# Kernel optimization log

Hardware: AMD Instinct MI355X
Metric: run time of the kernel (lower is better)

Reference implementation:

```python
import jax, jax.numpy as jnp
import numpy as np
import math

T, B = 512, 32
QD, SD, H, NH = 128, 256, 512, 8
NQ, NS, NSUB = 30000, 400, 8
DKEY = QD + 2 * SD      # 640
DVAL = 4 * SD + QD      # 1152
P = H + 2 * SD + QD     # 1152 (pred_in_feature)
DH = H // NH            # 64
NEG = -1e32


def _layernorm(x, g, b, eps=1e-5):
    mu = jnp.mean(x, axis=-1, keepdims=True)
    var = jnp.mean((x - mu) ** 2, axis=-1, keepdims=True)
    return (x - mu) * jax.lax.rsqrt(var + eps) * g + b


def setup_inputs() -> dict:
    key = jax.random.key(0)
    ks = iter(jax.random.split(key, 48))
    def nrm(shape, scale=0.05):
        return (scale * jax.random.normal(next(ks), shape)).astype(jnp.float32)
    inp = {}
    inp['ans'] = jax.random.randint(next(ks), (T, B), 1, 5, dtype=jnp.int32)
    inp['correct_ans'] = jax.random.randint(next(ks), (T, B), 1, 5, dtype=jnp.int32)
    inp['labels'] = jax.random.randint(next(ks), (T, B), 0, 2, dtype=jnp.int32)
    inp['mask'] = jnp.ones((T, B), jnp.float32)
    inp['q_ids'] = jax.random.randint(next(ks), (T, B), 0, NQ, dtype=jnp.int32)
    inp['subject_ids'] = jax.random.randint(next(ks), (T, B, NSUB), 0, NS, dtype=jnp.int32)
    inp['subject_mask'] = (jax.random.uniform(next(ks), (T, B, NSUB)) < 0.7).astype(jnp.float32)
    inp['Eq'] = nrm((NQ, QD)); inp['Es'] = nrm((NS, SD))
    inp['Ea'] = nrm((4, SD)); inp['El'] = nrm((2, SD))
    inp['Wq'] = nrm((H, DKEY)); inp['bq'] = jnp.zeros((H,), jnp.float32)
    inp['Wk'] = nrm((H, DKEY)); inp['bk'] = jnp.zeros((H,), jnp.float32)
    inp['Wv'] = nrm((H, DVAL)); inp['bv'] = jnp.zeros((H,), jnp.float32)
    inp['Wo'] = nrm((H, H)); inp['bo'] = jnp.zeros((H,), jnp.float32)
    inp['ln1_g'] = jnp.ones((H,), jnp.float32); inp['ln1_b'] = jnp.zeros((H,), jnp.float32)
    inp['W1'] = nrm((H, H)); inp['b1'] = jnp.zeros((H,), jnp.float32)
    inp['W2'] = nrm((H, H)); inp['b2'] = jnp.zeros((H,), jnp.float32)
    inp['ln2_g'] = jnp.ones((H,), jnp.float32); inp['ln2_b'] = jnp.zeros((H,), jnp.float32)
    inp['gammas'] = jnp.zeros((NH, 1, 1), jnp.float32)
    inp['L1W'] = nrm((P, P)); inp['L1b'] = jnp.zeros((P,), jnp.float32)
    inp['L2W'] = nrm((P, P)); inp['L2b'] = jnp.zeros((P,), jnp.float32)
    inp['OW'] = nrm((1, P)); inp['Ob'] = jnp.zeros((1,), jnp.float32)
    return inp


def _forward(ans, correct_ans, labels, q_ids, subject_ids,
             mask, subject_mask, Eq, Es, Ea, El,
             Wq, bq, Wk, bk, Wv, bv, Wo, bo, ln1_g, ln1_b,
             W1, b1, W2, b2, ln2_g, ln2_b, gammas,
             L1W, L1b, L2W, L2b, OW, Ob):
    m3 = mask[:, :, None]                                   # [T,B,1]
    subjects = jnp.sum(Es[subject_ids] * subject_mask[..., None], axis=2)   # [T,B,SD]
    questions = Eq[q_ids]                                   # [T,B,QD]
    ans_embed = Ea[ans - 1] * m3
    ca_embed = Ea[correct_ans - 1]
    lab_embed = El[labels] * m3
    query = jnp.concatenate([questions, subjects, ca_embed], axis=-1)       # [T,B,DKEY]
    value = jnp.concatenate([lab_embed, ans_embed, ca_embed, questions, subjects], axis=-1)  # [T,B,DVAL]
    # note: original applies q_linear to kk and k_linear to qq (qq==kk==query here); akt=True => no pos-embed
    q = (query @ Wq.T + bq).reshape(T, B, NH, DH).transpose(1, 2, 0, 3)     # [B,NH,T,DH]
    k = (query @ Wk.T + bk).reshape(T, B, NH, DH).transpose(1, 2, 0, 3)
    v = (value @ Wv.T + bv).reshape(T, B, NH, DH).transpose(1, 2, 0, 3)
    scores = jnp.einsum('bhqd,bhkd->bhqk', q, k) / math.sqrt(DH)            # [B,NH,T,T]
    scores = jnp.where(mask.T[:, None, None, :] == 0, NEG, scores)
    # exponential distance decay (Softplus-gamma), applied AFTER the key-pad fill as in the original
    idx = jnp.arange(T)
    pe = jnp.sqrt(jnp.abs(idx[None, :] - idx[:, None]).astype(jnp.float32)) # [T,T]
    total_effect = jnp.clip(jnp.exp(pe[None] * (-jax.nn.softplus(gammas))), 1e-5, 1e5)  # [NH,T,T]
    scores = scores * total_effect[None]
    causal_bad = jnp.triu(jnp.ones((T, T), bool))            # upper incl. diagonal is masked
    scores = jnp.where(causal_bad, NEG, scores)
    scores = jax.nn.softmax(scores, axis=-1)
    scores = scores.at[:, :, 0, :].set(0.0)                  # pad-zero first query row
    attn = jnp.einsum('bhqk,bhkd->bhqd', scores, v)
    concat = attn.transpose(2, 0, 1, 3).reshape(T, B, H)
    out = _layernorm(concat @ Wo.T + bo, ln1_g, ln1_b)
    ffn = jax.nn.relu(out @ W1.T + b1) @ W2.T + b2
    out = out + _layernorm(ffn, ln2_g, ln2_b)
    pred = jnp.concatenate([out, questions, subjects, ca_embed], axis=-1)   # [T,B,P]
    h = jax.nn.relu(pred @ L1W.T + L1b)
    h = jax.nn.relu(h @ L2W.T + L2b)
    logits = ((h + pred) @ OW.T + Ob)[..., 0]                # [T,B]
    y = labels.astype(jnp.float32)
    bce = jnp.maximum(logits, 0.0) - logits * y + jnp.log1p(jnp.exp(-jnp.abs(logits)))
    loss = jnp.mean(bce * mask) / jnp.mean(mask)
    return loss


def reference(ans, correct_ans, labels, mask, q_ids, subject_ids, subject_mask,
              Eq, Es, Ea, El, Wq, bq, Wk, bk, Wv, bv, Wo, bo, ln1_g, ln1_b,
              W1, b1, W2, b2, ln2_g, ln2_b, gammas, L1W, L1b, L2W, L2b, OW, Ob):
    return _forward(ans, correct_ans, labels, q_ids, subject_ids,
                    mask, subject_mask, Eq, Es, Ea, El,
                    Wq, bq, Wk, bk, Wv, bv, Wo, bo, ln1_g, ln1_b,
                    W1, b1, W2, b2, ln2_g, ln2_b, gammas,
                    L1W, L1b, L2W, L2b, OW, Ob)
```

## Files before the change

kernel.cpp:

```cpp
#include <hip/hip_runtime.h>
#include <math.h>

#define T_LEN 512
#define B_SZ  32
#define NHEAD 8
#define DHEAD 64
#define H_DIM 512
#define TBTOK 16384
#define P_DIM 1152
#define P_PAD 1280

typedef unsigned short ushort_t;
typedef short short8 __attribute__((ext_vector_type(8)));
typedef float f32x4 __attribute__((ext_vector_type(4)));

__device__ __forceinline__ ushort_t f2bf(float f) {
    union { float f; unsigned int u; } v; v.f = f;
    unsigned int r = v.u + 0x7fffu + ((v.u >> 16) & 1u);
    return (ushort_t)(r >> 16);
}
__device__ __forceinline__ float bf2f(ushort_t h) {
    union { unsigned int u; float f; } v; v.u = ((unsigned int)h) << 16;
    return v.f;
}
__device__ __forceinline__ void gload_lds16(const void* g, void* l) {
    __builtin_amdgcn_global_load_lds(
        (const __attribute__((address_space(1))) void*)g,
        (__attribute__((address_space(3))) void*)l, 16, 0, 0);
}

__global__ __launch_bounds__(256) void convert_weights(
    const float* __restrict__ wq, const float* __restrict__ wk,
    const float* __restrict__ wv, const float* __restrict__ wo,
    const float* __restrict__ w1, const float* __restrict__ w2,
    ushort_t* __restrict__ dst, float* __restrict__ accum)
{
    if (blockIdx.x == 0 && threadIdx.x < 2) accum[threadIdx.x] = 0.f;
    const unsigned int offs[7] = {0u, 327680u, 655360u, 1245184u, 1507328u,
                                  1769472u, 2031616u};
    unsigned int c = (blockIdx.x * 256 + threadIdx.x) * 4;
    const float* srcs[6] = {wq, wk, wv, wo, w1, w2};
    int s = 0;
#pragma unroll
    for (int i = 0; i < 5; i++) s += (c >= offs[i + 1]) ? 1 : 0;
    float4 v = *(const float4*)(srcs[s] + (c - offs[s]));
    ushort4 o;
    o.x = f2bf(v.x); o.y = f2bf(v.y); o.z = f2bf(v.z); o.w = f2bf(v.w);
    *(ushort4*)(dst + c) = o;
}

__global__ __launch_bounds__(256) void pad_weights(
    const float* __restrict__ l1, const float* __restrict__ l2,
    const float* __restrict__ L1b, const float* __restrict__ L2b,
    const float* __restrict__ OW,
    ushort_t* __restrict__ l1d, ushort_t* __restrict__ l2d,
    float* __restrict__ L1bp, float* __restrict__ L2bp, float* __restrict__ OWp)
{
    int blk = blockIdx.x;
    if (blk < 1440) {
        int o4 = (blk * 256 + threadIdx.x) * 4;
        int row = o4 / 1152;
        int col = o4 - row * 1152;
        ushort4 o; o.x = 0; o.y = 0; o.z = 0; o.w = 0;
        if (row < 1152) {
            float4 v = *(const float4*)(l1 + (size_t)row * 1152 + col);
            o.x = f2bf(v.x); o.y = f2bf(v.y); o.z = f2bf(v.z); o.w = f2bf(v.w);
        }
        *(ushort4*)(l1d + o4) = o;
    } else if (blk < 3040) {
        int o4 = ((blk - 1440) * 256 + threadIdx.x) * 4;
        int row = o4 / 1280;
        int col = o4 - row * 1280;
        ushort4 o; o.x = 0; o.y = 0; o.z = 0; o.w = 0;
        if (row < 1152 && col < 1152) {
            float4 v = *(const float4*)(l2 + (size_t)row * 1152 + col);
            o.x = f2bf(v.x); o.y = f2bf(v.y); o.z = f2bf(v.z); o.w = f2bf(v.w);
        }
        *(ushort4*)(l2d + o4) = o;
    } else {
        for (int i = threadIdx.x; i < P_PAD; i += 256) {
            L1bp[i] = (i < P_DIM) ? L1b[i] : 0.f;
            L2bp[i] = (i < P_DIM) ? L2b[i] : 0.f;
            OWp[i]  = (i < P_DIM) ? OW[i]  : 0.f;
        }
    }
}

__global__ __launch_bounds__(256) void embed_kernel(
    const int* __restrict__ ans, const int* __restrict__ cans,
    const int* __restrict__ labels, const float* __restrict__ mask,
    const int* __restrict__ qids, const int* __restrict__ sids,
    const float* __restrict__ smask,
    const float* __restrict__ Eq, const float* __restrict__ Es,
    const float* __restrict__ Ea, const float* __restrict__ El,
    ushort_t* __restrict__ pred_bf, ushort_t* __restrict__ value_bf,
    const float* __restrict__ OW, const float* __restrict__ Ob,
    float* __restrict__ lgits)
{
    __shared__ float red[4];
    int m = blockIdx.x;
    int tid = threadIdx.x;
    float mval = mask[m];
    int qid = qids[m];
    int a   = ans[m] - 1;
    int ca  = cans[m] - 1;
    int lb  = labels[m];
    ushort_t* pr = pred_bf  + (size_t)m * P_DIM;
    ushort_t* vr = value_bf + (size_t)m * P_DIM;

    float part = 0.f;
    if (tid < 128) {
        ushort_t qv = f2bf(Eq[(size_t)qid * 128 + tid]);
        pr[512 + tid] = qv;
        vr[768 + tid] = qv;
        part = bf2f(qv) * OW[512 + tid];
    }
    int d = tid;
    float s = 0.f;
#pragma unroll
    for (int j = 0; j < 8; j++) {
        int  sid = sids[m * 8 + j];
        float sm = smask[m * 8 + j];
        s += Es[(size_t)sid * 256 + d] * sm;
    }
    ushort_t sb = f2bf(s);
    pr[640 + d] = sb;
    vr[896 + d] = sb;
    ushort_t cab = f2bf(Ea[ca * 256 + d]);
    pr[896 + d] = cab;
    vr[512 + d] = cab;
    vr[256 + d] = f2bf(Ea[a * 256 + d] * mval);
    vr[0   + d] = f2bf(El[lb * 256 + d] * mval);

    part = fmaf(bf2f(sb),  OW[640 + d], part);
    part = fmaf(bf2f(cab), OW[896 + d], part);
#pragma unroll
    for (int off = 32; off >= 1; off >>= 1) part += __shfl_xor(part, off, 64);
    if ((tid & 63) == 0) red[tid >> 6] = part;
    __syncthreads();
    if (tid == 0) lgits[m] = red[0] + red[1] + red[2] + red[3] + Ob[0];
}

template<int MODE, bool RELU>
__global__ __launch_bounds__(256) void mgemm(
    const ushort_t* __restrict__ A, int lda,
    const ushort_t* __restrict__ W, int ldw,
    const float* __restrict__ bias, const float* __restrict__ bias2,
    ushort_t* __restrict__ Cb, ushort_t* __restrict__ Cb2, int ldc, int K,
    const float* __restrict__ OW, float* __restrict__ lg)
{
    __shared__ __align__(16) ushort_t As[128 * 32];
    __shared__ __align__(16) ushort_t Ws[128 * 32];
    __shared__ __align__(16) ushort_t et[4][32][72];

    const int m0 = blockIdx.x * 128;
    const int n0 = blockIdx.y * 128;
    const int tid  = threadIdx.x;
    const int wave = tid >> 6;
    const int lane = tid & 63;
    const int wm = wave & 1, wn = wave >> 1;

    f32x4 acc[4][4] = {};

    const int srow = lane >> 2;
    const int lchunk = ((((lane & 3) - ((srow >> 1) & 3)) & 3)) * 8;
    int arowA, arowB;
    if (MODE == 4) {
        int mA = m0 + wave * 32 + srow;
        int mB = mA + 16;
        arowA = ((mA & 511) << 5) + (mA >> 9);
        arowB = ((mB & 511) << 5) + (mB >> 9);
    } else {
        arowA = m0 + wave * 32 + srow;
        arowB = arowA + 16;
    }
    const ushort_t* Ag0 = A + (size_t)arowA * lda + lchunk;
    const ushort_t* Ag1 = A + (size_t)arowB * lda + lchunk;
    const ushort_t* Wg0 = W + (size_t)(n0 + wave * 32 + srow) * ldw + lchunk;
    const ushort_t* Wg1 = Wg0 + (size_t)16 * ldw;
    ushort_t* Al0 = &As[(wave * 32) * 32];
    ushort_t* Al1 = &As[(wave * 32 + 16) * 32];
    ushort_t* Wl0 = &Ws[(wave * 32) * 32];
    ushort_t* Wl1 = &Ws[(wave * 32 + 16) * 32];

    const int fr   = lane & 15;
    const int quad = lane >> 4;
    const int csw  = ((quad + ((fr >> 1) & 3)) & 3) * 8;

    for (int k0 = 0; k0 < K; k0 += 32) {
        gload_lds16(Ag0 + k0, Al0);
        gload_lds16(Ag1 + k0, Al1);
        gload_lds16(Wg0 + k0, Wl0);
        gload_lds16(Wg1 + k0, Wl1);
        __syncthreads();
        short8 af[4], wf[4];
#pragma unroll
        for (int i = 0; i < 4; i++)
            af[i] = *(const short8*)&As[(wm * 64 + i * 16 + fr) * 32 + csw];
#pragma unroll
        for (int j = 0; j < 4; j++)
            wf[j] = *(const short8*)&Ws[(wn * 64 + j * 16 + fr) * 32 + csw];
#pragma unroll
        for (int i = 0; i < 4; i++)
#pragma unroll
            for (int j = 0; j < 4; j++)
                acc[i][j] = __builtin_amdgcn_mfma_f32_16x16x32_bf16(
                    af[i], wf[j], acc[i][j], 0, 0, 0);
        __syncthreads();
    }

    const int nbase = n0 + wn * 64;
    bool side = (MODE == 5) && (nbase >= 512);
    const float* bp = side ? bias2 : bias;
    const int boff  = (MODE == 5) ? (nbase & 511) : nbase;
    const float scl = (MODE == 5 && !side) ? 0.125f : 1.f;

    const int sub8 = (lane & 7) * 8;
    const int grp  = lane >> 3;

#pragma unroll
    for (int hh = 0; hh < 2; hh++) {
        if (MODE == 4) {
#pragma unroll
            for (int i = 0; i < 4; i++)
#pragma unroll
                for (int r = 0; r < 4; r++) {
                    int rl = i * 16 + quad * 4 + r;
#pragma unroll
                    for (int j = 2 * hh; j < 2 * hh + 2; j++) {
                        int cl = j * 16 + fr;
                        float v = acc[i][j][r] + bp[boff + cl];
                        if (RELU) v = fmaxf(v, 0.f);
                        et[wave][cl - 32 * hh][rl] = f2bf(v);
                    }
                }
        } else {
#pragma unroll
            for (int i = 2 * hh; i < 2 * hh + 2; i++)
#pragma unroll
                for (int r = 0; r < 4; r++) {
                    int rl = i * 16 + quad * 4 + r;
#pragma unroll
                    for (int j = 0; j < 4; j++) {
                        int cl = j * 16 + fr;
                        float v = (acc[i][j][r] + bp[boff + cl]) * scl;
                        if (RELU) v = fmaxf(v, 0.f);
                        et[wave][rl - 32 * hh][cl] = f2bf(v);
                    }
                }
        }
#pragma unroll
        for (int rr = 0; rr < 4; rr++) {
            int rowl = rr * 8 + grp;
            short8 val = *(const short8*)&et[wave][rowl][sub8];
            if (MODE == 1) {
                int row = m0 + wm * 64 + 32 * hh + rowl;
                int col = nbase + sub8;
                *(short8*)&Cb[(size_t)row * ldc + col] = val;
            } else if (MODE == 5) {
                int row = m0 + wm * 64 + 32 * hh + rowl;
                int t = row >> 5, b = row & 31;
                int h = (nbase >> 6) & 7;
                ushort_t* base = side ? Cb2 : Cb;
                *(short8*)&base[(((size_t)(b * 8 + h)) << 15) + ((size_t)t << 6) + sub8] = val;
            } else {
                int m = m0 + wm * 64 + sub8;
                int b = m >> 9, t = m & 511;
                int h = nbase >> 6;
                int d = 32 * hh + rowl;
                *(short8*)&Cb[(((size_t)(b * 8 + h)) << 15) + ((size_t)d << 9) + t] = val;
            }
        }
    }
}

template<int MODE, bool RELU>
__global__ __launch_bounds__(512, 2) void gemm320(
    const ushort_t* __restrict__ A, int lda,
    const ushort_t* __restrict__ W, int ldw,
    const float* __restrict__ bias,
    ushort_t* __restrict__ Cb, int ldc, int K,
    const float* __restrict__ OW, float* __restrict__ lg)
{
    __shared__ __align__(16) ushort_t As2[2][2][256 * 32];
    __shared__ __align__(16) ushort_t Bs2[2][2][320 * 32];

    const int m0 = blockIdx.x * 256;
    const int n0 = blockIdx.y * 320;
    const int tid  = threadIdx.x;
    const int wave = tid >> 6;
    const int lane = tid & 63;
    const int wm = wave >> 2, wn = wave & 3;
    const int fr   = lane & 15;
    const int quad = lane >> 4;
    const int csw  = ((quad + ((fr >> 1) & 3)) & 3) * 8;

    const int slr = lane >> 2;
    const int sc  = (((lane & 3) - ((lane >> 3) & 3)) & 3) * 8;
    const ushort_t* Asrc = A + (size_t)(m0 + slr) * lda + sc;
    const ushort_t* Wsrc = W + (size_t)(n0 + slr) * ldw + sc;
    const int NT = K >> 6;

    auto stA = [&](int t, int kh) {
#pragma unroll
        for (int n = 0; n < 2; n++) {
            int rl = (wave + 8 * n) << 4;
            gload_lds16(Asrc + (size_t)rl * lda + (t * 64 + kh * 32),
                        &As2[t & 1][kh][rl * 32]);
        }
    };
    auto stB = [&](int t, int kh) {
#pragma unroll
        for (int n = 0; n < 2; n++) {
            int rl = (wave + 8 * n) << 4;
            gload_lds16(Wsrc + (size_t)rl * ldw + (t * 64 + kh * 32),
                        &Bs2[t & 1][kh][rl * 32]);
        }
        if (wave < 4) {
            int rl = (wave + 16) << 4;
            gload_lds16(Wsrc + (size_t)rl * ldw + (t * 64 + kh * 32),
                        &Bs2[t & 1][kh][rl * 32]);
        }
    };
    auto waitK = [&](int t) {
        if (t + 2 < NT) {
            if (wave < 4) asm volatile("s_waitcnt vmcnt(5)" ::: "memory");
            else          asm volatile("s_waitcnt vmcnt(4)" ::: "memory");
        } else {
            asm volatile("s_waitcnt vmcnt(0)" ::: "memory");
        }
    };

    f32x4 acc[8][5] = {};

    stA(0, 0); stB(0, 0); stA(0, 1); stB(0, 1);
    if (NT > 1) { stA(1, 0); stB(1, 0); }
    if (NT > 2) {
        if (wave < 4) asm volatile("s_waitcnt vmcnt(5)" ::: "memory");
        else          asm volatile("s_waitcnt vmcnt(4)" ::: "memory");
    } else {
        asm volatile("s_waitcnt vmcnt(0)" ::: "memory");
    }
    __builtin_amdgcn_s_barrier();

    short8 af[4], bf[5];
    for (int t = 0; t < NT; ++t) {
        const int db = t & 1;
        const ushort_t* Ar0 = &As2[db][0][0];
        const ushort_t* Ar1 = &As2[db][1][0];
        const ushort_t* Br0 = &Bs2[db][0][0];
        const ushort_t* Br1 = &Bs2[db][1][0];

#pragma unroll
        for (int i = 0; i < 4; i++)
            af[i] = *(const short8*)&Ar0[(wm * 128 + i * 16 + fr) * 32 + csw];
#pragma unroll
        for (int j = 0; j < 5; j++)
            bf[j] = *(const short8*)&Br0[(wn * 80 + j * 16 + fr) * 32 + csw];
        if (t + 1 < NT) stA(t + 1, 1);
        __builtin_amdgcn_s_barrier();
        __builtin_amdgcn_s_setprio(1);
#pragma unroll
        for (int i = 0; i < 4; i++)
#pragma unroll
            for (int j = 0; j < 5; j++)
                acc[i][j] = __builtin_amdgcn_mfma_f32_16x16x32_bf16(
                    af[i], bf[j], acc[i][j], 0, 0, 0);
        __builtin_amdgcn_s_setprio(0);
        __builtin_amdgcn_s_barrier();

#pragma unroll
        for (int i = 0; i < 4; i++)
            af[i] = *(const short8*)&Ar0[(wm * 128 + 64 + i * 16 + fr) * 32 + csw];
        if (t + 1 < NT) stB(t + 1, 1);
        __builtin_amdgcn_s_barrier();
        __builtin_amdgcn_s_setprio(1);
#pragma unroll
        for (int i = 0; i < 4; i++)
#pragma unroll
            for (int j = 0; j < 5; j++)
                acc[4 + i][j] = __builtin_amdgcn_mfma_f32_16x16x32_bf16(
                    af[i], bf[j], acc[4 + i][j], 0, 0, 0);
        __builtin_amdgcn_s_setprio(0);
        __builtin_amdgcn_s_barrier();

#pragma unroll
        for (int i = 0; i < 4; i++)
            af[i] = *(const short8*)&Ar1[(wm * 128 + i * 16 + fr) * 32 + csw];
#pragma unroll
        for (int j = 0; j < 5; j++)
            bf[j] = *(const short8*)&Br1[(wn * 80 + j * 16 + fr) * 32 + csw];
        if (t + 2 < NT) stA(t + 2, 0);
        __builtin_amdgcn_s_barrier();
        __builtin_amdgcn_s_setprio(1);
#pragma unroll
        for (int i = 0; i < 4; i++)
#pragma unroll
            for (int j = 0; j < 5; j++)
                acc[i][j] = __builtin_amdgcn_mfma_f32_16x16x32_bf16(
                    af[i], bf[j], acc[i][j], 0, 0, 0);
        __builtin_amdgcn_s_setprio(0);
        __builtin_amdgcn_s_barrier();

#pragma unroll
        for (int i = 0; i < 4; i++)
            af[i] = *(const short8*)&Ar1[(wm * 128 + 64 + i * 16 + fr) * 32 + csw];
        if (t + 2 < NT) stB(t + 2, 0);
        waitK(t);
        __builtin_amdgcn_s_barrier();
        __builtin_amdgcn_s_setprio(1);
#pragma unroll
        for (int i = 0; i < 4; i++)
#pragma unroll
            for (int j = 0; j < 5; j++)
                acc[4 + i][j] = __builtin_amdgcn_mfma_f32_16x16x32_bf16(
                    af[i], bf[j], acc[4 + i][j], 0, 0, 0);
        __builtin_amdgcn_s_setprio(0);
        __builtin_amdgcn_s_barrier();
    }

    const int nbase = n0 + wn * 80;

    if (MODE == 3) {
#pragma unroll
        for (int ii = 0; ii < 8; ii++)
#pragma unroll
            for (int r = 0; r < 4; r++) {
                int row = m0 + wm * 128 + (ii >> 2) * 64 + (ii & 3) * 16 + quad * 4 + r;
                float part = 0.f;
#pragma unroll
                for (int j = 0; j < 5; j++) {
                    int col = nbase + j * 16 + fr;
                    float v = fmaxf(acc[ii][j][r] + bias[col], 0.f);
                    part = fmaf(v, OW[col], part);
                }
                part += __shfl_xor(part, 1, 64);
                part += __shfl_xor(part, 2, 64);
                part += __shfl_xor(part, 4, 64);
                part += __shfl_xor(part, 8, 64);
                if (fr == 0) atomicAdd(&lg[row], part);
            }
        return;
    }

    ushort_t* etw = ((ushort_t*)As2) + wave * (16 * 88);
#pragma unroll
    for (int ii = 0; ii < 8; ii++) {
#pragma unroll
        for (int r = 0; r < 4; r++)
#pragma unroll
            for (int j = 0; j < 5; j++) {
                float v = acc[ii][j][r] + bias[nbase + j * 16 + fr];
                if (RELU) v = fmaxf(v, 0.f);
                etw[(quad * 4 + r) * 88 + j * 16 + fr] = f2bf(v);
            }
        int rowb = m0 + wm * 128 + (ii >> 2) * 64 + (ii & 3) * 16;
        for (int u = lane; u < 160; u += 64) {
            int rr = u / 10;
            int cc = u - rr * 10;
            short8 val = *(const short8*)&etw[rr * 88 + cc * 8];
            *(short8*)&Cb[(size_t)(rowb + rr) * ldc + nbase + cc * 8] = val;
        }
    }
}

__global__ __launch_bounds__(256) void attn_mfma(
    const ushort_t* __restrict__ qb, const ushort_t* __restrict__ kb,
    const ushort_t* __restrict__ vtb, const float* __restrict__ mask,
    const float* __restrict__ gammas, ushort_t* __restrict__ attnc)
{
    __shared__ __align__(16) ushort_t kbuf[2][64 * 64];
    __shared__ __align__(16) ushort_t vbuf[2][64 * 64];
    __shared__ __align__(16) ushort_t ps[4][16][72];
    __shared__ float decayF[512];
    __shared__ float mneg[512];

    const int bh  = blockIdx.x;
    const int b   = bh >> 3;
    const int h   = bh & 7;
    const int qt0 = (7 - blockIdx.y) * 64;
    const int tid  = threadIdx.x;
    const int wave = tid >> 6;
    const int lane = tid & 63;
    const int fr   = lane & 15;
    const int quad = lane >> 4;

    {
        float g  = gammas[h];
        float sp = (g > 20.f) ? g : log1pf(expf(g));
        for (int i = tid; i < 512; i += 256) {
            decayF[i] = fmaxf(exp2f(-sp * 1.44269504f * sqrtf((float)i)), 1e-5f)
                        * 1.44269504f;
            mneg[i]   = (mask[(size_t)i * B_SZ + b] == 0.f) ? -1e32f : 0.f;
        }
    }

    const int qr0 = qt0 + wave * 16;
    const ushort_t* qbase = qb  + ((size_t)bh << 15);
    const ushort_t* kbase = kb  + ((size_t)bh << 15);
    const ushort_t* vbase = vtb + ((size_t)bh << 15);

    short8 af0 = *(const short8*)(qbase + (size_t)(qr0 + fr) * 64 + quad * 8);
    short8 af1 = *(const short8*)(qbase + (size_t)(qr0 + fr) * 64 + 32 + quad * 8);
    const short8 ones = {0x3F80, 0x3F80, 0x3F80, 0x3F80,
                         0x3F80, 0x3F80, 0x3F80, 0x3F80};

    const int rl0 = wave * 16 + (lane >> 3);
    const int rl1 = rl0 + 8;
    const int sc0 = (((lane & 7) - rl0) & 7) * 8;
    const int sc1 = (((lane & 7) - rl1) & 7) * 8;

    auto stage = [&](int kt, int bufi) {
        gload_lds16(kbase + (size_t)(kt + rl0) * 64 + sc0, &kbuf[bufi][(wave * 16) * 64]);
        gload_lds16(kbase + (size_t)(kt + rl1) * 64 + sc1, &kbuf[bufi][(wave * 16 + 8) * 64]);
        gload_lds16(vbase + (size_t)rl0 * T_LEN + kt + sc0, &vbuf[bufi][(wave * 16) * 64]);
        gload_lds16(vbase + (size_t)rl1 * T_LEN + kt + sc1, &vbuf[bufi][(wave * 16 + 8) * 64]);
    };
    auto frag = [&](const ushort_t* buf, int row, int lchunk) -> short8 {
        return *(const short8*)&buf[row * 64 + ((lchunk + row) & 7) * 8];
    };

    stage(0, 0);

    f32x4 o[4] = {};
    f32x4 lacc = {};
    int bufi = 0;

    for (int kt0 = 0; kt0 <= qt0; kt0 += 64) {
        __syncthreads();
        if (kt0 < qt0) stage(kt0 + 64, bufi ^ 1);
        const bool diag = (kt0 == qt0);
        const ushort_t* kb_ = kbuf[bufi];
        const ushort_t* vb_ = vbuf[bufi];

        f32x4 sacc[4] = {};
#pragma unroll
        for (int j = 0; j < 4; j++) {
            int row = j * 16 + fr;
            short8 k0 = frag(kb_, row, quad);
            short8 k1 = frag(kb_, row, quad + 4);
            sacc[j] = __builtin_amdgcn_mfma_f32_16x16x32_bf16(af0, k0, sacc[j], 0, 0, 0);
            sacc[j] = __builtin_amdgcn_mfma_f32_16x16x32_bf16(af1, k1, sacc[j], 0, 0, 0);
        }

#pragma unroll
        for (int j = 0; j < 4; j++) {
            int kg = kt0 + j * 16 + fr;
            float mn = mneg[kg];
            int qgb = qr0 + quad * 4;
            if (!diag) {
                int base = qgb - kg;
#pragma unroll
                for (int r = 0; r < 4; r++) {
                    float t = fmaf(sacc[j][r], decayF[base + r], mn);
                    union { float f; unsigned u; } cv; cv.f = exp2f(t);
                    ps[wave][quad * 4 + r][j * 16 + fr] = (ushort_t)(cv.u >> 16);
                }
            } else {
#pragma unroll
                for (int r = 0; r < 4; r++) {
                    int didx = qgb + r - kg;
                    float dec = decayF[didx > 0 ? didx : 0];
                    float t = fmaf(sacc[j][r], dec, mn);
                    if (didx <= 0) t = -1e32f;
                    union { float f; unsigned u; } cv; cv.f = exp2f(t);
                    ps[wave][quad * 4 + r][j * 16 + fr] = (ushort_t)(cv.u >> 16);
                }
            }
        }
        short8 pf0 = *(const short8*)&ps[wave][fr][quad * 8];
        short8 pf1 = *(const short8*)&ps[wave][fr][32 + quad * 8];
        lacc = __builtin_amdgcn_mfma_f32_16x16x32_bf16(pf0, ones, lacc, 0, 0, 0);
        lacc = __builtin_amdgcn_mfma_f32_16x16x32_bf16(pf1, ones, lacc, 0, 0, 0);
#pragma unroll
        for (int j2 = 0; j2 < 4; j2++) {
            int row = j2 * 16 + fr;
            short8 v0 = frag(vb_, row, quad);
            short8 v1 = frag(vb_, row, quad + 4);
            o[j2] = __builtin_amdgcn_mfma_f32_16x16x32_bf16(pf0, v0, o[j2], 0, 0, 0);
            o[j2] = __builtin_amdgcn_mfma_f32_16x16x32_bf16(pf1, v1, o[j2], 0, 0, 0);
        }
        bufi ^= 1;
    }

#pragma unroll
    for (int r = 0; r < 4; r++) {
        int qg = qr0 + quad * 4 + r;
        float linv = (qg == 0) ? 0.f : 1.f / lacc[r];
#pragma unroll
        for (int j2 = 0; j2 < 4; j2++)
            ps[wave][quad * 4 + r][j2 * 16 + fr] = f2bf(o[j2][r] * linv);
    }
    const int sub8 = (lane & 7) * 8;
    const int grp  = lane >> 3;
#pragma unroll
    for (int half = 0; half < 2; half++) {
        int rowl = half * 8 + grp;
        short8 val = *(const short8*)&ps[wave][rowl][sub8];
        int qg = qr0 + rowl;
        *(short8*)&attnc[((size_t)qg * B_SZ + b) * H_DIM + h * DHEAD + sub8] = val;
    }
}

__global__ __launch_bounds__(256) void ln1_kernel(
    const ushort_t* __restrict__ X, const float* __restrict__ g,
    const float* __restrict__ bta, ushort_t* __restrict__ Yb)
{
    int m    = blockIdx.x * 4 + (threadIdx.x >> 6);
    int lane = threadIdx.x & 63;
    int c0   = lane * 8;
    const ushort_t* xr = X + (size_t)m * H_DIM + c0;
    float x[8];
    float s = 0.f, ss = 0.f;
    short8 xv = *(const short8*)xr;
#pragma unroll
    for (int i = 0; i < 8; i++) {
        x[i] = bf2f((ushort_t)xv[i]);
        s += x[i]; ss += x[i] * x[i];
    }
#pragma unroll
    for (int off = 32; off >= 1; off >>= 1) {
        s  += __shfl_xor(s,  off, 64);
        ss += __shfl_xor(ss, off, 64);
    }
    float mu  = s * (1.f / 512.f);
    float var = ss * (1.f / 512.f) - mu * mu;
    float rs  = rsqrtf(var + 1e-5f);
    ushort_t yb[8];
#pragma unroll
    for (int i = 0; i < 8; i++)
        yb[i] = f2bf((x[i] - mu) * rs * g[c0 + i] + bta[c0 + i]);
    *(short8*)(Yb + (size_t)m * H_DIM + c0) = *(short8*)&yb[0];
}

__global__ __launch_bounds__(256) void ln2_kernel(
    const ushort_t* __restrict__ X, const float* __restrict__ g,
    const float* __restrict__ bta, const ushort_t* __restrict__ res,
    ushort_t* __restrict__ pred_bf, const float* __restrict__ OW,
    float* __restrict__ lg)
{
    int m    = blockIdx.x * 4 + (threadIdx.x >> 6);
    int lane = threadIdx.x & 63;
    int c0   = lane * 8;
    const ushort_t* xr = X + (size_t)m * H_DIM + c0;
    float x[8];
    float s = 0.f, ss = 0.f;
    short8 xv = *(const short8*)xr;
#pragma unroll
    for (int i = 0; i < 8; i++) {
        x[i] = bf2f((ushort_t)xv[i]);
        s += x[i]; ss += x[i] * x[i];
    }
#pragma unroll
    for (int off = 32; off >= 1; off >>= 1) {
        s  += __shfl_xor(s,  off, 64);
        ss += __shfl_xor(ss, off, 64);
    }
    float mu  = s * (1.f / 512.f);
    float var = ss * (1.f / 512.f) - mu * mu;
    float rs  = rsqrtf(var + 1e-5f);
    short8 rv = *(const short8*)(res + (size_t)m * H_DIM + c0);
    ushort_t yb[8];
    float part = 0.f;
#pragma unroll
    for (int i = 0; i < 8; i++) {
        float v = (x[i] - mu) * rs * g[c0 + i] + bta[c0 + i] + bf2f((ushort_t)rv[i]);
        yb[i] = f2bf(v);
        part = fmaf(v, OW[c0 + i], part);
    }
    *(short8*)(pred_bf + (size_t)m * P_DIM + c0) = *(short8*)&yb[0];
#pragma unroll
    for (int off = 32; off >= 1; off >>= 1) part += __shfl_xor(part, off, 64);
    if (lane == 0) lg[m] += part;
}

__global__ __launch_bounds__(256) void bce_kernel(
    const float* __restrict__ lg, const int* __restrict__ labels,
    const float* __restrict__ mask, float* __restrict__ accum)
{
    int m    = blockIdx.x * 256 + threadIdx.x;
    int lane = threadIdx.x & 63;
    float l  = lg[m];
    float y  = (float)labels[m];
    float mv = mask[m];
    float a  = (fmaxf(l, 0.f) - l * y + log1pf(expf(-fabsf(l)))) * mv;
#pragma unroll
    for (int off = 32; off >= 1; off >>= 1) {
        a  += __shfl_xor(a,  off, 64);
        mv += __shfl_xor(mv, off, 64);
    }
    if (lane == 0) {
        atomicAdd(accum,     a);
        atomicAdd(accum + 1, mv);
    }
}

__global__ void finalize_kernel(const float* __restrict__ accum, float* __restrict__ out)
{
    out[0] = accum[0] / accum[1];
}

extern "C" void kernel_launch(void* const* d_in, const int* in_sizes, int n_in,
                              void* d_out, int out_size, void* d_ws, size_t ws_size,
                              hipStream_t stream)
{
    (void)in_sizes; (void)n_in; (void)out_size;
    const int*   ans    = (const int*)  d_in[0];
    const int*   cans   = (const int*)  d_in[1];
    const int*   labels = (const int*)  d_in[2];
    const float* mask   = (const float*)d_in[3];
    const int*   qids   = (const int*)  d_in[4];
    const int*   sids   = (const int*)  d_in[5];
    const float* smask  = (const float*)d_in[6];
    const float* Eq     = (const float*)d_in[7];
    const float* Es     = (const float*)d_in[8];
    const float* Ea     = (const float*)d_in[9];
    const float* El     = (const float*)d_in[10];
    const float* Wq     = (const float*)d_in[11];
    const float* bq     = (const float*)d_in[12];
    const float* Wk     = (const float*)d_in[13];
    const float* bk     = (const float*)d_in[14];
    const float* Wv     = (const float*)d_in[15];
    const float* bv     = (const float*)d_in[16];
    const float* Wo     = (const float*)d_in[17];
    const float* bo     = (const float*)d_in[18];
    const float* ln1_g  = (const float*)d_in[19];
    const float* ln1_b  = (const float*)d_in[20];
    const float* W1     = (const float*)d_in[21];
    const float* b1     = (const float*)d_in[22];
    const float* W2     = (const float*)d_in[23];
    const float* b2     = (const float*)d_in[24];
    const float* ln2_g  = (const float*)d_in[25];
    const float* ln2_b  = (const float*)d_in[26];
    const float* gammas = (const float*)d_in[27];
    const float* L1W    = (const float*)d_in[28];
    const float* L1b    = (const float*)d_in[29];
    const float* L2W    = (const float*)d_in[30];
    const float* L2b    = (const float*)d_in[31];
    const float* OW     = (const float*)d_in[32];
    const float* Ob     = (const float*)d_in[33];
    float* out = (float*)d_out;

    const size_t U = (size_t)TBTOK * 64;
    if (ws_size < 42 * U * sizeof(float)) return;
    float* ws = (float*)d_ws;
    ushort_t* wtb      = (ushort_t*)(ws);
    ushort_t* pred_bf  = (ushort_t*)(ws + 3 * U);
    ushort_t* value_bf = (ushort_t*)(ws + 12 * U);
    ushort_t* qb       = (ushort_t*)(ws + 21 * U);
    ushort_t* kb       = (ushort_t*)(ws + 25 * U);
    ushort_t* vtb      = (ushort_t*)(ws + 29 * U);
    ushort_t* attnc_bf = (ushort_t*)(ws + 33 * U);
    ushort_t* x1_bf    = (ushort_t*)(ws + 12 * U);
    ushort_t* out1_bf  = (ushort_t*)(ws + 24 * U);
    ushort_t* f1_bf    = (ushort_t*)(ws + 28 * U);
    ushort_t* f2_bf    = (ushort_t*)(ws + 32 * U);
    ushort_t* h1_bf    = (ushort_t*)(ws + 12 * U);
    float*    lgits    = ws + 41 * U;
    float*    accum    = lgits + TBTOK;
    float*    OWp      = accum + 2;
    float*    L1bp     = OWp + P_PAD;
    float*    L2bp     = L1bp + P_PAD;

    ushort_t* wqk_b = wtb + 0;
    ushort_t* wv_b  = wtb + 655360;
    ushort_t* wo_b  = wtb + 1245184;
    ushort_t* w1_b  = wtb + 1507328;
    ushort_t* w2_b  = wtb + 1769472;
    ushort_t* l1_b  = wtb + 2031616;
    ushort_t* l2_b  = wtb + 3506176;

    convert_weights<<<1984, 256, 0, stream>>>(Wq, Wk, Wv, Wo, W1, W2, wtb, accum);
    pad_weights<<<3041, 256, 0, stream>>>(L1W, L2W, L1b, L2b, OW,
                                          l1_b, l2_b, L1bp, L2bp, OWp);
    embed_kernel<<<TBTOK, 256, 0, stream>>>(ans, cans, labels, mask, qids, sids,
                                            smask, Eq, Es, Ea, El, pred_bf, value_bf,
                                            OW, Ob, lgits);
    mgemm<5,false><<<dim3(TBTOK/128, 8), 256, 0, stream>>>(
        pred_bf + 512, P_DIM, wqk_b, 640, bq, bk, qb, kb, 0, 640, nullptr, nullptr);
    mgemm<4,false><<<dim3(TBTOK/128, 4), 256, 0, stream>>>(
        value_bf, P_DIM, wv_b, P_DIM, bv, nullptr, vtb, nullptr, 0, P_DIM, nullptr, nullptr);
    attn_mfma<<<dim3(B_SZ * NHEAD, 8), 256, 0, stream>>>(
        qb, kb, vtb, mask, gammas, attnc_bf);
    mgemm<1,false><<<dim3(TBTOK/128, 4), 256, 0, stream>>>(
        attnc_bf, H_DIM, wo_b, H_DIM, bo, nullptr, x1_bf, nullptr, H_DIM, H_DIM, nullptr, nullptr);
    ln1_kernel<<<TBTOK/4, 256, 0, stream>>>(x1_bf, ln1_g, ln1_b, out1_bf);
    mgemm<1,true><<<dim3(TBTOK/128, 4), 256, 0, stream>>>(
        out1_bf, H_DIM, w1_b, H_DIM, b1, nullptr, f1_bf, nullptr, H_DIM, H_DIM, nullptr, nullptr);
    mgemm<1,false><<<dim3(TBTOK/128, 4), 256, 0, stream>>>(
        f1_bf, H_DIM, w2_b, H_DIM, b2, nullptr, f2_bf, nullptr, H_DIM, H_DIM, nullptr, nullptr);
    ln2_kernel<<<TBTOK/4, 256, 0, stream>>>(f2_bf, ln2_g, ln2_b, out1_bf, pred_bf, OW, lgits);
    gemm320<1,true><<<dim3(TBTOK/256, P_PAD/320), 512, 0, stream>>>(
        pred_bf, P_DIM, l1_b, P_DIM, L1bp, h1_bf, P_PAD, P_DIM, nullptr, nullptr);
    gemm320<3,true><<<dim3(TBTOK/256, P_PAD/320), 512, 0, stream>>>(
        h1_bf, P_PAD, l2_b, P_PAD, L2bp, nullptr, 0, P_PAD, OWp, lgits);
    bce_kernel<<<TBTOK/256, 256, 0, stream>>>(lgits, labels, mask, accum);
    finalize_kernel<<<1, 1, 0, stream>>>(accum, out);
}
```

Measured before the change: 443.6 us.

## Replace simple 128x128 GEMMs with templated double-buffered 256-row pipelined GEMM

Generalises the pipelined 256xN gemm320 kernel into a template gemm4p parameterised by column tiles, and routes the QK, V, Wo, FFN and prediction-head GEMMs through it instead of the single-buffered 128x128 mgemm. The new kernel prefetches K tiles with vmcnt-based waits, uses setprio around MFMA bursts, and adds epilogues for the Q/K head-split layout and the transposed V layout. This aims to hide global-load latency and raise MFMA utilisation. The trade-off is fewer blocks per GEMM (64x4 grids), which can leave CUs idle, plus higher register and LDS pressure.

Measured after the change: 425.3 us. 1.04x faster.

```diff
diff --git a/kernel.cpp b/kernel.cpp
--- a/kernel.cpp
+++ b/kernel.cpp
@@ -141,152 +141,20 @@
     if (tid == 0) lgits[m] = red[0] + red[1] + red[2] + red[3] + Ob[0];
 }
 
-template<int MODE, bool RELU>
-__global__ __launch_bounds__(256) void mgemm(
+template<int JC, int MODE, bool RELU>
+__global__ __launch_bounds__(512, 2) void gemm4p(
     const ushort_t* __restrict__ A, int lda,
     const ushort_t* __restrict__ W, int ldw,
     const float* __restrict__ bias, const float* __restrict__ bias2,
     ushort_t* __restrict__ Cb, ushort_t* __restrict__ Cb2, int ldc, int K,
     const float* __restrict__ OW, float* __restrict__ lg)
 {
-    __shared__ __align__(16) ushort_t As[128 * 32];
-    __shared__ __align__(16) ushort_t Ws[128 * 32];
-    __shared__ __align__(16) ushort_t et[4][32][72];
-
-    const int m0 = blockIdx.x * 128;
-    const int n0 = blockIdx.y * 128;
-    const int tid  = threadIdx.x;
-    const int wave = tid >> 6;
-    const int lane = tid & 63;
-    const int wm = wave & 1, wn = wave >> 1;
-
-    f32x4 acc[4][4] = {};
-
-    const int srow = lane >> 2;
-    const int lchunk = ((((lane & 3) - ((srow >> 1) & 3)) & 3)) * 8;
-    int arowA, arowB;
-    if (MODE == 4) {
-        int mA = m0 + wave * 32 + srow;
-        int mB = mA + 16;
-        arowA = ((mA & 511) << 5) + (mA >> 9);
-        arowB = ((mB & 511) << 5) + (mB >> 9);
-    } else {
-        arowA = m0 + wave * 32 + srow;
-        arowB = arowA + 16;
-    }
-    const ushort_t* Ag0 = A + (size_t)arowA * lda + lchunk;
-    const ushort_t* Ag1 = A + (size_t)arowB * lda + lchunk;
-    const ushort_t* Wg0 = W + (size_t)(n0 + wave * 32 + srow) * ldw + lchunk;
-    const ushort_t* Wg1 = Wg0 + (size_t)16 * ldw;
-    ushort_t* Al0 = &As[(wave * 32) * 32];
-    ushort_t* Al1 = &As[(wave * 32 + 16) * 32];
-    ushort_t* Wl0 = &Ws[(wave * 32) * 32];
-    ushort_t* Wl1 = &Ws[(wave * 32 + 16) * 32];
-
-    const int fr   = lane & 15;
-    const int quad = lane >> 4;
-    const int csw  = ((quad + ((fr >> 1) & 3)) & 3) * 8;
-
-    for (int k0 = 0; k0 < K; k0 += 32) {
-        gload_lds16(Ag0 + k0, Al0);
-        gload_lds16(Ag1 + k0, Al1);
-        gload_lds16(Wg0 + k0, Wl0);
-        gload_lds16(Wg1 + k0, Wl1);
-        __syncthreads();
-        short8 af[4], wf[4];
-#pragma unroll
-        for (int i = 0; i < 4; i++)
-            af[i] = *(const short8*)&As[(wm * 64 + i * 16 + fr) * 32 + csw];
-#pragma unroll
-        for (int j = 0; j < 4; j++)
-            wf[j] = *(const short8*)&Ws[(wn * 64 + j * 16 + fr) * 32 + csw];
-#pragma unroll
-        for (int i = 0; i < 4; i++)
-#pragma unroll
-            for (int j = 0; j < 4; j++)
-                acc[i][j] = __builtin_amdgcn_mfma_f32_16x16x32_bf16(
-                    af[i], wf[j], acc[i][j], 0, 0, 0);
-        __syncthreads();
-    }
-
-    const int nbase = n0 + wn * 64;
-    bool side = (MODE == 5) && (nbase >= 512);
-    const float* bp = side ? bias2 : bias;
-    const int boff  = (MODE == 5) ? (nbase & 511) : nbase;
-    const float scl = (MODE == 5 && !side) ? 0.125f : 1.f;
-
-    const int sub8 = (lane & 7) * 8;
-    const int grp  = lane >> 3;
-
-#pragma unroll
-    for (int hh = 0; hh < 2; hh++) {
-        if (MODE == 4) {
-#pragma unroll
-            for (int i = 0; i < 4; i++)
-#pragma unroll
-                for (int r = 0; r < 4; r++) {
-                    int rl = i * 16 + quad * 4 + r;
-#pragma unroll
-                    for (int j = 2 * hh; j < 2 * hh + 2; j++) {
-                        int cl = j * 16 + fr;
-                        float v = acc[i][j][r] + bp[boff + cl];
-                        if (RELU) v = fmaxf(v, 0.f);
-                        et[wave][cl - 32 * hh][rl] = f2bf(v);
-                    }
-                }
-        } else {
-#pragma unroll
-            for (int i = 2 * hh; i < 2 * hh + 2; i++)
-#pragma unroll
-                for (int r = 0; r < 4; r++) {
-                    int rl = i * 16 + quad * 4 + r;
-#pragma unroll
-                    for (int j = 0; j < 4; j++) {
-                        int cl = j * 16 + fr;
-                        float v = (acc[i][j][r] + bp[boff + cl]) * scl;
-                        if (RELU) v = fmaxf(v, 0.f);
-                        et[wave][rl - 32 * hh][cl] = f2bf(v);
-                    }
-                }
-        }
-#pragma unroll
-        for (int rr = 0; rr < 4; rr++) {
-            int rowl = rr * 8 + grp;
-            short8 val = *(const short8*)&et[wave][rowl][sub8];
-            if (MODE == 1) {
-                int row = m0 + wm * 64 + 32 * hh + rowl;
-                int col = nbase + sub8;
-                *(short8*)&Cb[(size_t)row * ldc + col] = val;
-            } else if (MODE == 5) {
-                int row = m0 + wm * 64 + 32 * hh + rowl;
-                int t = row >> 5, b = row & 31;
-                int h = (nbase >> 6) & 7;
-                ushort_t* base = side ? Cb2 : Cb;
-                *(short8*)&base[(((size_t)(b * 8 + h)) << 15) + ((size_t)t << 6) + sub8] = val;
-            } else {
-                int m = m0 + wm * 64 + sub8;
-                int b = m >> 9, t = m & 511;
-                int h = nbase >> 6;
-                int d = 32 * hh + rowl;
-                *(short8*)&Cb[(((size_t)(b * 8 + h)) << 15) + ((size_t)d << 9) + t] = val;
-            }
-        }
-    }
-}
-
-template<int MODE, bool RELU>
-__global__ __launch_bounds__(512, 2) void gemm320(
-    const ushort_t* __restrict__ A, int lda,
-    const ushort_t* __restrict__ W, int ldw,
-    const float* __restrict__ bias,
-    ushort_t* __restrict__ Cb, int ldc, int K,
-    const float* __restrict__ OW, float* __restrict__ lg)
-{
+    constexpr int BN = JC * 64;
     __shared__ __align__(16) ushort_t As2[2][2][256 * 32];
-    __shared__ __align__(16) ushort_t Bs2[2][2][320 * 32];
+    __shared__ __align__(16) ushort_t Bs2[2][2][BN * 32];
 
     const int m0 = blockIdx.x * 256;
-    const int n0 = blockIdx.y * 320;
+    const int n0 = blockIdx.y * BN;
     const int tid  = threadIdx.x;
     const int wave = tid >> 6;
     const int lane = tid & 63;
@@ -297,7 +165,15 @@
 
     const int slr = lane >> 2;
     const int sc  = (((lane & 3) - ((lane >> 3) & 3)) & 3) * 8;
-    const ushort_t* Asrc = A + (size_t)(m0 + slr) * lda + sc;
+    const ushort_t* Asrc;
+    size_t aRS;
+    if (MODE == 4) {
+        Asrc = A + ((size_t)(((m0 & 511) + slr) << 5) + (m0 >> 9)) * lda + sc;
+        aRS  = (size_t)32 * lda;
+    } else {
+        Asrc = A + (size_t)(m0 + slr) * lda + sc;
+        aRS  = (size_t)lda;
+    }
     const ushort_t* Wsrc = W + (size_t)(n0 + slr) * ldw + sc;
     const int NT = K >> 6;
 
@@ -305,45 +181,43 @@
 #pragma unroll
         for (int n = 0; n < 2; n++) {
             int rl = (wave + 8 * n) << 4;
-            gload_lds16(Asrc + (size_t)rl * lda + (t * 64 + kh * 32),
+            gload_lds16(Asrc + (size_t)rl * aRS + (t * 64 + kh * 32),
                         &As2[t & 1][kh][rl * 32]);
         }
     };
     auto stB = [&](int t, int kh) {
 #pragma unroll
-        for (int n = 0; n < 2; n++) {
+        for (int n = 0; n < JC / 2; n++) {
             int rl = (wave + 8 * n) << 4;
             gload_lds16(Wsrc + (size_t)rl * ldw + (t * 64 + kh * 32),
                         &Bs2[t & 1][kh][rl * 32]);
         }
-        if (wave < 4) {
-            int rl = (wave + 16) << 4;
-            gload_lds16(Wsrc + (size_t)rl * ldw + (t * 64 + kh * 32),
-                        &Bs2[t & 1][kh][rl * 32]);
+        if (JC & 1) {
+            if (wave < 4) {
+                int rl = (wave + 8 * (JC / 2)) << 4;
+                gload_lds16(Wsrc + (size_t)rl * ldw + (t * 64 + kh * 32),
+                            &Bs2[t & 1][kh][rl * 32]);
+            }
         }
     };
-    auto waitK = [&](int t) {
-        if (t + 2 < NT) {
+    auto waitSteady = [&]() {
+        if (JC == 2)      asm volatile("s_waitcnt vmcnt(3)" ::: "memory");
+        else if (JC == 4) asm volatile("s_waitcnt vmcnt(4)" ::: "memory");
+        else {
             if (wave < 4) asm volatile("s_waitcnt vmcnt(5)" ::: "memory");
             else          asm volatile("s_waitcnt vmcnt(4)" ::: "memory");
-        } else {
-            asm volatile("s_waitcnt vmcnt(0)" ::: "memory");
         }
     };
 
-    f32x4 acc[8][5] = {};
+    f32x4 acc[8][JC] = {};
 
     stA(0, 0); stB(0, 0); stA(0, 1); stB(0, 1);
     if (NT > 1) { stA(1, 0); stB(1, 0); }
-    if (NT > 2) {
-        if (wave < 4) asm volatile("s_waitcnt vmcnt(5)" ::: "memory");
-        else          asm volatile("s_waitcnt vmcnt(4)" ::: "memory");
-    } else {
-        asm volatile("s_waitcnt vmcnt(0)" ::: "memory");
-    }
+    if (NT > 2) waitSteady();
+    else        asm volatile("s_waitcnt vmcnt(0)" ::: "memory");
     __builtin_amdgcn_s_barrier();
 
-    short8 af[4], bf[5];
+    short8 af[4], bf[JC];
     for (int t = 0; t < NT; ++t) {
         const int db = t & 1;
         const ushort_t* Ar0 = &As2[db][0][0];
@@ -355,15 +229,15 @@
         for (int i = 0; i < 4; i++)
             af[i] = *(const short8*)&Ar0[(wm * 128 + i * 16 + fr) * 32 + csw];
 #pragma unroll
-        for (int j = 0; j < 5; j++)
-            bf[j] = *(const short8*)&Br0[(wn * 80 + j * 16 + fr) * 32 + csw];
+        for (int j = 0; j < JC; j++)
+            bf[j] = *(const short8*)&Br0[(wn * (JC * 16) + j * 16 + fr) * 32 + csw];
         if (t + 1 < NT) stA(t + 1, 1);
         __builtin_amdgcn_s_barrier();
         __builtin_amdgcn_s_setprio(1);
 #pragma unroll
         for (int i = 0; i < 4; i++)
 #pragma unroll
-            for (int j = 0; j < 5; j++)
+            for (int j = 0; j < JC; j++)
                 acc[i][j] = __builtin_amdgcn_mfma_f32_16x16x32_bf16(
                     af[i], bf[j], acc[i][j], 0, 0, 0);
         __builtin_amdgcn_s_setprio(0);
@@ -378,7 +252,7 @@
 #pragma unroll
         for (int i = 0; i < 4; i++)
 #pragma unroll
-            for (int j = 0; j < 5; j++)
+            for (int j = 0; j < JC; j++)
                 acc[4 + i][j] = __builtin_amdgcn_mfma_f32_16x16x32_bf16(
                     af[i], bf[j], acc[4 + i][j], 0, 0, 0);
         __builtin_amdgcn_s_setprio(0);
@@ -388,15 +262,15 @@
         for (int i = 0; i < 4; i++)
             af[i] = *(const short8*)&Ar1[(wm * 128 + i * 16 + fr) * 32 + csw];
 #pragma unroll
-        for (int j = 0; j < 5; j++)
-            bf[j] = *(const short8*)&Br1[(wn * 80 + j * 16 + fr) * 32 + csw];
+        for (int j = 0; j < JC; j++)
+            bf[j] = *(const short8*)&Br1[(wn * (JC * 16) + j * 16 + fr) * 32 + csw];
         if (t + 2 < NT) stA(t + 2, 0);
         __builtin_amdgcn_s_barrier();
         __builtin_amdgcn_s_setprio(1);
 #pragma unroll
         for (int i = 0; i < 4; i++)
 #pragma unroll
-            for (int j = 0; j < 5; j++)
+            for (int j = 0; j < JC; j++)
                 acc[i][j] = __builtin_amdgcn_mfma_f32_16x16x32_bf16(
                     af[i], bf[j], acc[i][j], 0, 0, 0);
         __builtin_amdgcn_s_setprio(0);
@@ -406,20 +280,21 @@
         for (int i = 0; i < 4; i++)
             af[i] = *(const short8*)&Ar1[(wm * 128 + 64 + i * 16 + fr) * 32 + csw];
         if (t + 2 < NT) stB(t + 2, 0);
-        waitK(t);
+        if (t + 2 < NT) waitSteady();
+        else            asm volatile("s_waitcnt vmcnt(0)" ::: "memory");
         __builtin_amdgcn_s_barrier();
         __builtin_amdgcn_s_setprio(1);
 #pragma unroll
         for (int i = 0; i < 4; i++)
 #pragma unroll
-            for (int j = 0; j < 5; j++)
+            for (int j = 0; j < JC; j++)
                 acc[4 + i][j] = __builtin_amdgcn_mfma_f32_16x16x32_bf16(
                     af[i], bf[j], acc[4 + i][j], 0, 0, 0);
         __builtin_amdgcn_s_setprio(0);
         __builtin_amdgcn_s_barrier();
     }
 
-    const int nbase = n0 + wn * 80;
+    const int nbase = n0 + wn * (JC * 16);
 
     if (MODE == 3) {
 #pragma unroll
@@ -429,7 +304,7 @@
                 int row = m0 + wm * 128 + (ii >> 2) * 64 + (ii & 3) * 16 + quad * 4 + r;
                 float part = 0.f;
 #pragma unroll
-                for (int j = 0; j < 5; j++) {
+                for (int j = 0; j < JC; j++) {
                     int col = nbase + j * 16 + fr;
                     float v = fmaxf(acc[ii][j][r] + bias[col], 0.f);
                     part = fmaf(v, OW[col], part);
@@ -443,23 +318,89 @@
         return;
     }
 
-    ushort_t* etw = ((ushort_t*)As2) + wave * (16 * 88);
-#pragma unroll
-    for (int ii = 0; ii < 8; ii++) {
-#pragma unroll
-        for (int r = 0; r < 4; r++)
-#pragma unroll
-            for (int j = 0; j < 5; j++) {
-                float v = acc[ii][j][r] + bias[nbase + j * 16 + fr];
-                if (RELU) v = fmaxf(v, 0.f);
-                etw[(quad * 4 + r) * 88 + j * 16 + fr] = f2bf(v);
+    if (MODE == 5) {
+        bool side = (nbase >= 512);
+        const float* bp = side ? bias2 : bias;
+        const int boff  = nbase & 511;
+        const float scl = side ? 1.f : 0.125f;
+        ushort_t* base  = side ? Cb2 : Cb;
+        const int h = (nbase >> 6) & 7;
+        ushort_t* etw = ((ushort_t*)As2) + wave * (16 * 72);
+#pragma unroll
+        for (int ii = 0; ii < 8; ii++) {
+#pragma unroll
+            for (int r = 0; r < 4; r++)
+#pragma unroll
+                for (int j = 0; j < 4; j++) {
+                    float v = (acc[ii][j][r] + bp[boff + j * 16 + fr]) * scl;
+                    etw[(quad * 4 + r) * 72 + j * 16 + fr] = f2bf(v);
+                }
+            int rowb = m0 + wm * 128 + (ii >> 2) * 64 + (ii & 3) * 16;
+#pragma unroll
+            for (int u = lane; u < 128; u += 64) {
+                int rr = u >> 3, cc = (u & 7) * 8;
+                int row = rowb + rr;
+                int tq = row >> 5, b = row & 31;
+                short8 val = *(const short8*)&etw[rr * 72 + cc];
+                *(short8*)&base[(((size_t)(b * 8 + h)) << 15) + ((size_t)tq << 6) + cc] = val;
             }
-        int rowb = m0 + wm * 128 + (ii >> 2) * 64 + (ii & 3) * 16;
-        for (int u = lane; u < 160; u += 64) {
-            int rr = u / 10;
-            int cc = u - rr * 10;
-            short8 val = *(const short8*)&etw[rr * 88 + cc * 8];
-            *(short8*)&Cb[(size_t)(rowb + rr) * ldc + nbase + cc * 8] = val;
+        }
+        return;
+    }
+
+    if (MODE == 4) {
+        ushort_t* etw = ((ushort_t*)As2) + wave * (32 * 72);
+        const int h = nbase >> 6;
+        const int dbase = nbase & 63;
+#pragma unroll
+        for (int mh = 0; mh < 2; mh++) {
+#pragma unroll
+            for (int i = 0; i < 4; i++)
+#pragma unroll
+                for (int r = 0; r < 4; r++) {
+                    int rl = i * 16 + quad * 4 + r;
+#pragma unroll
+                    for (int j = 0; j < 2; j++) {
+                        int cl = j * 16 + fr;
+                        float v = acc[mh * 4 + i][j][r] + bias[nbase + cl];
+                        etw[cl * 72 + rl] = f2bf(v);
+                    }
+                }
+            int mbase = m0 + wm * 128 + mh * 64;
+            int b = mbase >> 9, t0 = mbase & 511;
+            size_t obase = (((size_t)(b * 8 + h)) << 15) + ((size_t)dbase << 9) + t0;
+#pragma unroll
+            for (int u = lane; u < 256; u += 64) {
+                int dr = u >> 3, cc = (u & 7) * 8;
+                short8 val = *(const short8*)&etw[dr * 72 + cc];
+                *(short8*)&Cb[obase + ((size_t)dr << 9) + cc] = val;
+            }
+        }
+        return;
+    }
+
+    {
+        constexpr int STR = JC * 16 + 8;
+        constexpr int CPR = 2 * JC;
+        ushort_t* etw = ((ushort_t*)As2) + wave * (16 * STR);
+#pragma unroll
+        for (int ii = 0; ii < 8; ii++) {
+#pragma unroll
+            for (int r = 0; r < 4; r++)
+#pragma unroll
+                for (int j = 0; j < JC; j++) {
+                    float v = acc[ii][j][r] + bias[nbase + j * 16 + fr];
+                    if (RELU) v = fmaxf(v, 0.f);
+                    etw[(quad * 4 + r) * STR + j * 16 + fr] = f2bf(v);
+                }
+            int rowb = m0 + wm * 128 + (ii >> 2) * 64 + (ii & 3) * 16;
+#pragma unroll
+            for (int u = lane; u < 16 * CPR; u += 64) {
+                int rr = u / CPR;
+                int cc = u - rr * CPR;
+                short8 val = *(const short8*)&etw[rr * STR + cc * 8];
+                *(short8*)&Cb[(size_t)(rowb + rr) * ldc + nbase + cc * 8] = val;
+            }
         }
     }
 }
@@ -776,24 +717,24 @@
     embed_kernel<<<TBTOK, 256, 0, stream>>>(ans, cans, labels, mask, qids, sids,
                                             smask, Eq, Es, Ea, El, pred_bf, value_bf,
                                             OW, Ob, lgits);
-    mgemm<5,false><<<dim3(TBTOK/128, 8), 256, 0, stream>>>(
+    gemm4p<4,5,false><<<dim3(64, 4), 512, 0, stream>>>(
         pred_bf + 512, P_DIM, wqk_b, 640, bq, bk, qb, kb, 0, 640, nullptr, nullptr);
-    mgemm<4,false><<<dim3(TBTOK/128, 4), 256, 0, stream>>>(
+    gemm4p<2,4,false><<<dim3(64, 4), 512, 0, stream>>>(
         value_bf, P_DIM, wv_b, P_DIM, bv, nullptr, vtb, nullptr, 0, P_DIM, nullptr, nullptr);
     attn_mfma<<<dim3(B_SZ * NHEAD, 8), 256, 0, stream>>>(
         qb, kb, vtb, mask, gammas, attnc_bf);
-    mgemm<1,false><<<dim3(TBTOK/128, 4), 256, 0, stream>>>(
+    gemm4p<2,1,false><<<dim3(64, 4), 512, 0, stream>>>(
         attnc_bf, H_DIM, wo_b, H_DIM, bo, nullptr, x1_bf, nullptr, H_DIM, H_DIM, nullptr, nullptr);
     ln1_kernel<<<TBTOK/4, 256, 0, stream>>>(x1_bf, ln1_g, ln1_b, out1_bf);
-    mgemm<1,true><<<dim3(TBTOK/128, 4), 256, 0, stream>>>(
+    gemm4p<2,1,true><<<dim3(64, 4), 512, 0, stream>>>(
         out1_bf, H_DIM, w1_b, H_DIM, b1, nullptr, f1_bf, nullptr, H_DIM, H_DIM, nullptr, nullptr);
-    mgemm<1,false><<<dim3(TBTOK/128, 4), 256, 0, stream>>>(
+    gemm4p<2,1,false><<<dim3(64, 4), 512, 0, stream>>>(
         f1_bf, H_DIM, w2_b, H_DIM, b2, nullptr, f2_bf, nullptr, H_DIM, H_DIM, nullptr, nullptr);
     ln2_kernel<<<TBTOK/4, 256, 0, stream>>>(f2_bf, ln2_g, ln2_b, out1_bf, pred_bf, OW, lgits);
-    gemm320<1,true><<<dim3(TBTOK/256, P_PAD/320), 512, 0, stream>>>(
-        pred_bf, P_DIM, l1_b, P_DIM, L1bp, h1_bf, P_PAD, P_DIM, nullptr, nullptr);
-    gemm320<3,true><<<dim3(TBTOK/256, P_PAD/320), 512, 0, stream>>>(
-        h1_bf, P_PAD, l2_b, P_PAD, L2bp, nullptr, 0, P_PAD, OWp, lgits);
+    gemm4p<5,1,true><<<dim3(64, 4), 512, 0, stream>>>(
+        pred_bf, P_DIM, l1_b, P_DIM, L1bp, nullptr, h1_bf, nullptr, P_PAD, P_DIM, nullptr, nullptr);
+    gemm4p<5,3,true><<<dim3(64, 4), 512, 0, stream>>>(
+        h1_bf, P_PAD, l2_b, P_PAD, L2bp, nullptr, nullptr, nullptr, 0, P_PAD, OWp, lgits);
     bce_kernel<<<TBTOK/256, 256, 0, stream>>>(lgits, labels, mask, accum);
     finalize_kernel<<<1, 1, 0, stream>>>(accum, out);
 }
```
